# Performance work log

Hardware: AMD Instinct MI355X
Metric: run time of the kernel (lower is better)

The kernel has to match this reference:

```python
import jax, jax.numpy as jnp
import numpy as np

N_NODES = 100000
N_EDGES = 1250000
F_IN = 128
F_OUT = 64
N_GRAPHS = 256


def setup_inputs() -> dict:
    key = jax.random.key(0)
    k1, k2, k3, k4, k5 = jax.random.split(key, 5)
    node_feat = jax.random.normal(k1, (N_NODES, F_IN), dtype=jnp.float32)
    edge_index = jax.random.randint(k2, (2, N_EDGES), 0, N_NODES, dtype=jnp.int32)
    batch = jnp.sort(jax.random.randint(k3, (N_NODES,), 0, N_GRAPHS, dtype=jnp.int32))
    # PyG Linear weight layout: [out_channels, in_channels]; glorot-ish scale
    W = jax.random.normal(k4, (F_OUT, F_IN), dtype=jnp.float32) / np.sqrt(F_IN)
    b = jax.random.normal(k5, (F_OUT,), dtype=jnp.float32) * 0.01
    return {"node_feat": node_feat, "edge_index": edge_index, "batch": batch,
            "W": W, "b": b, "num_graphs": N_GRAPHS}


def reference(node_feat, edge_index, batch, W, b, num_graphs):
    n = node_feat.shape[0]
    # GCNConv: linear transform (no bias yet)
    x = node_feat @ W.T  # [N, F_OUT]
    # add self-loops (PyG default add_self_loops=True)
    loop = jnp.arange(n, dtype=edge_index.dtype)
    row = jnp.concatenate([edge_index[0], loop])  # source
    col = jnp.concatenate([edge_index[1], loop])  # target
    # symmetric normalization deg^{-1/2}[row] * deg^{-1/2}[col], deg over targets
    deg = jax.ops.segment_sum(jnp.ones_like(col, dtype=x.dtype), col, num_segments=n)
    dis = jnp.where(deg > 0, jax.lax.rsqrt(deg), 0.0)
    norm = dis[row] * dis[col]  # [E+N]
    # gather -> scale -> scatter-add, then bias
    agg = jax.ops.segment_sum(x[row] * norm[:, None], col, num_segments=n)
    out = jax.nn.relu(agg + b)
    # global_mean_pool over batch ids
    sums = jax.ops.segment_sum(out, batch, num_segments=num_graphs)
    counts = jax.ops.segment_sum(jnp.ones((n,), out.dtype), batch, num_segments=num_graphs)
    return sums / jnp.maximum(counts, 1.0)[:, None]
```

## Files before the change

### kernel.cpp

```cpp
#include <hip/hip_runtime.h>

#define N_NODES  100000
#define N_EDGES  1250000
#define F_IN     128
#define F_OUT    64
#define N_GRAPHS 256
#define NB_LIN   1563
#define NB_LINB  391
#define NBKT     782
#define NCHK     256
#define CHKSZ    4883
#define M_H      (NBKT * NCHK)
#define MB_H     196
#define BKT_CAP  2048

typedef __attribute__((ext_vector_type(8))) short short8;
typedef __attribute__((ext_vector_type(4))) float f32x4;

static __device__ __forceinline__ unsigned short f2bf(float f) {
    unsigned u = __builtin_bit_cast(unsigned, f);
    u += 0x7fff + ((u >> 16) & 1);
    return (unsigned short)(u >> 16);
}
static __device__ __forceinline__ float bf2f(unsigned short h) {
    unsigned u = ((unsigned)h) << 16;
    return __builtin_bit_cast(float, u);
}
static __device__ __forceinline__ float bflo(unsigned v) {
    return __builtin_bit_cast(float, v << 16);
}
static __device__ __forceinline__ float bfhi(unsigned v) {
    return __builtin_bit_cast(float, v & 0xffff0000u);
}

__global__ __launch_bounds__(256) void hist_k(const int* __restrict__ col,
                                              int* __restrict__ H) {
    __shared__ int cnt[NBKT];
    int c = blockIdx.x, tid = threadIdx.x;
    for (int b = tid; b < NBKT; b += 256) cnt[b] = 0;
    __syncthreads();
    int s = c * CHKSZ;
    int e = s + CHKSZ; if (e > N_EDGES) e = N_EDGES;
    for (int i = s + tid; i < e; i += 256)
        atomicAdd(&cnt[col[i] >> 7], 1);
    __syncthreads();
    for (int b = tid; b < NBKT; b += 256)
        H[b * NCHK + c] = cnt[b];
}

__global__ __launch_bounds__(1024) void scanH1_k(int* __restrict__ H, int* __restrict__ bsum) {
    __shared__ int lds[1024];
    int tid = threadIdx.x;
    int i = blockIdx.x * 1024 + tid;
    int v = (i < M_H) ? H[i] : 0;
    lds[tid] = v;
    __syncthreads();
    for (int off = 1; off < 1024; off <<= 1) {
        int t = (tid >= off) ? lds[tid - off] : 0;
        __syncthreads();
        lds[tid] += t;
        __syncthreads();
    }
    if (i < M_H) H[i] = lds[tid] - v;
    if (tid == 1023) bsum[blockIdx.x] = lds[tid];
}

__global__ __launch_bounds__(256) void scanH2_k(int* __restrict__ bsum) {
    __shared__ int lds[256];
    int tid = threadIdx.x;
    int v = (tid < MB_H) ? bsum[tid] : 0;
    lds[tid] = v;
    __syncthreads();
    for (int off = 1; off < 256; off <<= 1) {
        int t = (tid >= off) ? lds[tid - off] : 0;
        __syncthreads();
        lds[tid] += t;
        __syncthreads();
    }
    if (tid < MB_H) bsum[tid] = lds[tid] - v;
}

__global__ __launch_bounds__(1024) void scanH3_k(int* __restrict__ H, const int* __restrict__ bsum) {
    int i = blockIdx.x * 1024 + threadIdx.x;
    if (i < M_H) H[i] += bsum[blockIdx.x];
}

__global__ __launch_bounds__(256) void scatter_lin_k(const int* __restrict__ row,
                                                     const int* __restrict__ col,
                                                     const int* __restrict__ Hs,
                                                     int2* __restrict__ part,
                                                     const float* __restrict__ x,
                                                     const float* __restrict__ W,
                                                     unsigned short* __restrict__ z) {
    __shared__ unsigned smem[2 * 64 * 64];
    int tid = threadIdx.x;

    if (blockIdx.x < NCHK) {
        int* cur = (int*)smem;
        int c = blockIdx.x;
        for (int b = tid; b < NBKT; b += 256) cur[b] = Hs[b * NCHK + c];
        __syncthreads();
        int s = c * CHKSZ;
        int e = s + CHKSZ; if (e > N_EDGES) e = N_EDGES;
        for (int i = s + tid; i < e; i += 256) {
            int cc = col[i], rr = row[i];
            int p = atomicAdd(&cur[cc >> 7], 1);
            part[p] = make_int2(rr, cc);
        }
        return;
    }

    unsigned* xs = smem;
    unsigned* ws = smem + 64 * 64;
    int lb = blockIdx.x - NCHK;

    #pragma unroll
    for (int rr = 0; rr < 8; ++rr) {
        int idx = rr * 256 + tid;
        int n = idx >> 5, q = idx & 31;
        int d   = (n << 6) + (q << 1);
        int sdw = (n & 7) << 2;
        const float4 wv = *(const float4*)(W + (size_t)n * F_IN + q * 4);
        ws[(d ^ sdw)]     = (unsigned)f2bf(wv.x) | ((unsigned)f2bf(wv.y) << 16);
        ws[(d ^ sdw) + 1] = (unsigned)f2bf(wv.z) | ((unsigned)f2bf(wv.w) << 16);
    }

    int lane = tid & 63;
    int wv_  = tid >> 6;
    int m0   = wv_ << 4;
    int lr   = lane & 15;
    int lg   = lane >> 4;

    for (int t4 = 0; t4 < 4; ++t4) {
        int tile = lb * 4 + t4;
        if (tile >= NB_LIN) break;
        int base = tile * 64;
        int nmax = N_NODES - base; if (nmax > 64) nmax = 64;

        #pragma unroll
        for (int rr = 0; rr < 8; ++rr) {
            int idx = rr * 256 + tid;
            int n = idx >> 5, q = idx & 31;
            int d   = (n << 6) + (q << 1);
            int sdw = (n & 7) << 2;
            float4 xv = make_float4(0.f, 0.f, 0.f, 0.f);
            if (n < nmax) xv = *(const float4*)(x + (size_t)(base + n) * F_IN + q * 4);
            xs[(d ^ sdw)]     = (unsigned)f2bf(xv.x) | ((unsigned)f2bf(xv.y) << 16);
            xs[(d ^ sdw) + 1] = (unsigned)f2bf(xv.z) | ((unsigned)f2bf(xv.w) << 16);
        }
        __syncthreads();

        f32x4 acc0 = (f32x4)(0.f), acc1 = (f32x4)(0.f);
        f32x4 acc2 = (f32x4)(0.f), acc3 = (f32x4)(0.f);

        #pragma unroll
        for (int t = 0; t < 4; ++t) {
            int nn = m0 + lr;
            int da = ((nn << 6) + (t << 4) + (lg << 2)) ^ ((nn & 7) << 2);
            short8 a = *(const short8*)(xs + da);
            #pragma unroll
            for (int ff = 0; ff < 4; ++ff) {
                int f  = (ff << 4) + lr;
                int db = ((f << 6) + (t << 4) + (lg << 2)) ^ ((f & 7) << 2);
                short8 b = *(const short8*)(ws + db);
                f32x4 c = (ff == 0) ? acc0 : (ff == 1) ? acc1 : (ff == 2) ? acc2 : acc3;
                c = __builtin_amdgcn_mfma_f32_16x16x32_bf16(a, b, c, 0, 0, 0);
                if (ff == 0) acc0 = c; else if (ff == 1) acc1 = c;
                else if (ff == 2) acc2 = c; else acc3 = c;
            }
        }

        #pragma unroll
        for (int r = 0; r < 4; ++r) {
            int node = m0 + (lg << 2) + r;
            if (node < nmax) {
                size_t o = (size_t)(base + node) * F_OUT + lr;
                z[o +  0] = f2bf(acc0[r]);
                z[o + 16] = f2bf(acc1[r]);
                z[o + 32] = f2bf(acc2[r]);
                z[o + 48] = f2bf(acc3[r]);
            }
        }
        __syncthreads();
    }
}

__global__ __launch_bounds__(256) void csr_k(const int* __restrict__ Hs,
                                             const int2* __restrict__ part,
                                             int* __restrict__ bucketF,
                                             int* __restrict__ deg,
                                             int* __restrict__ offs,
                                             float* __restrict__ dis,
                                             unsigned* __restrict__ z32) {
    __shared__ int rowL[BKT_CAP];
    __shared__ int colL[BKT_CAP];
    __shared__ int cnt[128], offsL[128], curL[128], scanT[128];
    __shared__ float disL[128];
    int b = blockIdx.x, tid = threadIdx.x;
    int s = Hs[b * NCHK];
    int e = (b < NBKT - 1) ? Hs[(b + 1) * NCHK] : N_EDGES;
    int m = e - s;

    if (tid < 128) cnt[tid] = 0;
    __syncthreads();
    for (int i = tid; i < m; i += 256) {
        int2 pr = part[s + i];
        rowL[i] = pr.x;
        int cl = pr.y & 127;
        colL[i] = cl;
        atomicAdd(&cnt[cl], 1);
    }
    __syncthreads();
    if (tid < 128) scanT[tid] = cnt[tid];
    __syncthreads();
    for (int off = 1; off < 128; off <<= 1) {
        int v = (tid < 128 && tid >= off) ? scanT[tid - off] : 0;
        __syncthreads();
        if (tid < 128) scanT[tid] += v;
        __syncthreads();
    }
    if (tid < 128) {
        int ex = scanT[tid] - cnt[tid];
        offsL[tid] = ex;
        curL[tid]  = ex;
        float d = rsqrtf((float)cnt[tid] + 1.0f);
        disL[tid] = d;
        int node = b * 128 + tid;
        if (node < N_NODES) {
            deg[node]  = cnt[tid];
            offs[node] = s + ex;
            dis[node]  = d;
        }
    }
    __syncthreads();
    for (int i = tid; i < m; i += 256) {
        int cl = colL[i];
        int p = atomicAdd(&curL[cl], 1);
        bucketF[s + p] = rowL[i];
    }
    int node = tid >> 1, half = tid & 1;
    int gnode = b * 128 + node;
    if (gnode < N_NODES) {
        float d = disL[node];
        unsigned* zp = z32 + (size_t)gnode * 32 + half * 16;
        #pragma unroll
        for (int k = 0; k < 16; ++k) {
            unsigned v = zp[k];
            zp[k] = (unsigned)f2bf(d * bflo(v)) | ((unsigned)f2bf(d * bfhi(v)) << 16);
        }
    }
}

__global__ __launch_bounds__(256, 4) void gather_pool_k(const unsigned short* __restrict__ y,
                                                        const int* __restrict__ offs,
                                                        const int* __restrict__ deg,
                                                        const int* __restrict__ bucket,
                                                        const float* __restrict__ dis,
                                                        const int* __restrict__ batch,
                                                        const float* __restrict__ bias,
                                                        float* __restrict__ psum,
                                                        int* __restrict__ pcnt) {
    int lane = threadIdx.x & 63;
    int wid  = threadIdx.x >> 6;
    int i0   = (blockIdx.x * 4 + wid) * 8;
    int eo   = lane >> 5;
    int fp   = lane & 31;
    float bx = bias[2 * fp], by = bias[2 * fp + 1];
    const unsigned short* yb = y + 2 * fp;

    int   om = (lane < 8) ? offs[i0 + lane]  : 0;
    int   dm = (lane < 8) ? deg[i0 + lane]   : 0;
    float sm = (lane < 8) ? dis[i0 + lane]   : 0.f;
    int   gm = (lane < 8) ? batch[i0 + lane] : 0;

    float rx = 0.f, ry = 0.f;
    int cur = -1, runlen = 0;
    #pragma unroll
    for (int n = 0; n < 8; ++n) {
        int i = i0 + n;
        int s = __shfl(om, n);
        int e = s + __shfl(dm, n);

        unsigned sv = *(const unsigned*)(yb + (size_t)i * F_OUT);
        float ax = (eo == 0) ? bflo(sv) : 0.f;
        float ay = (eo == 0) ? bfhi(sv) : 0.f;

        for (int j = s; j < e; j += 16) {
            int rr[8];
            #pragma unroll
            for (int u = 0; u < 8; ++u) {
                int id = j + 2 * u + eo;
                rr[u] = bucket[(id < e) ? id : e - 1];
            }
            unsigned wv[8];
            #pragma unroll
            for (int u = 0; u < 8; ++u) {
                unsigned w = *(const unsigned*)(yb + (size_t)rr[u] * F_OUT);
                wv[u] = (j + 2 * u + eo < e) ? w : 0u;
            }
            #pragma unroll
            for (int u = 0; u < 8; ++u) {
                ax += bflo(wv[u]);
                ay += bfhi(wv[u]);
            }
        }
        ax += __shfl_xor(ax, 32);
        ay += __shfl_xor(ay, 32);

        float di = __shfl(sm, n);
        float vx = fmaxf(fmaf(di, ax, bx), 0.f);
        float vy = fmaxf(fmaf(di, ay, by), 0.f);
        int g = __shfl(gm, n);
        if (g != cur) {
            if (cur >= 0 && eo == 0) {
                atomicAdd(&psum[cur * F_OUT + 2 * fp],     rx);
                atomicAdd(&psum[cur * F_OUT + 2 * fp + 1], ry);
                if (lane == 0) atomicAdd(&pcnt[cur], runlen);
            }
            cur = g; rx = 0.f; ry = 0.f; runlen = 0;
        }
        rx += vx; ry += vy; runlen++;
    }
    if (cur >= 0 && eo == 0) {
        atomicAdd(&psum[cur * F_OUT + 2 * fp],     rx);
        atomicAdd(&psum[cur * F_OUT + 2 * fp + 1], ry);
        if (lane == 0) atomicAdd(&pcnt[cur], runlen);
    }
}

__global__ __launch_bounds__(256) void final_k(const float* __restrict__ psum,
                                               const int* __restrict__ pcnt,
                                               float* __restrict__ out) {
    int t = blockIdx.x * blockDim.x + threadIdx.x;
    if (t < N_GRAPHS * F_OUT) {
        int g = t >> 6;
        float c = (float)(pcnt[g] > 1 ? pcnt[g] : 1);
        out[t] = psum[t] / c;
    }
}

extern "C" void kernel_launch(void* const* d_in, const int* in_sizes, int n_in,
                              void* d_out, int out_size, void* d_ws, size_t ws_size,
                              hipStream_t stream) {
    const float* node_feat = (const float*)d_in[0];
    const int*   edges     = (const int*)d_in[1];
    const int*   batch     = (const int*)d_in[2];
    const float* W         = (const float*)d_in[3];
    const float* b         = (const float*)d_in[4];

    unsigned short* z = (unsigned short*)d_ws;
    int2*  part    = (int2*)(z + (size_t)N_NODES * F_OUT);
    int*   bucketF = (int*)(part + N_EDGES);
    int*   H       = bucketF + N_EDGES;
    int*   bsumH   = H + M_H;
    int*   deg     = bsumH + 256;
    int*   offs    = deg + N_NODES;
    float* dis     = (float*)(offs + N_NODES);
    float* psum    = dis + N_NODES;
    int*   pcnt    = (int*)(psum + N_GRAPHS * F_OUT);

    hipMemsetAsync(psum, 0, ((size_t)N_GRAPHS * F_OUT + N_GRAPHS) * 4, stream);

    const int* row = edges;
    const int* col = edges + N_EDGES;

    hist_k<<<NCHK, 256, 0, stream>>>(col, H);
    scanH1_k<<<MB_H, 1024, 0, stream>>>(H, bsumH);
    scanH2_k<<<1, 256, 0, stream>>>(bsumH);
    scanH3_k<<<MB_H, 1024, 0, stream>>>(H, bsumH);
    scatter_lin_k<<<NCHK + NB_LINB, 256, 0, stream>>>(row, col, H, part,
                                                      node_feat, W, z);
    csr_k<<<NBKT, 256, 0, stream>>>(H, part, bucketF, deg, offs, dis, (unsigned*)z);
    gather_pool_k<<<N_NODES / 32, 256, 0, stream>>>(z, offs, deg, bucketF,
                                                    dis, batch, b, psum, pcnt);
    final_k<<<(N_GRAPHS * F_OUT + 255) / 256, 256, 0, stream>>>(psum, pcnt, (float*)d_out);
}
```

Before: 118.8 us.

## Split feature matrix into four 16-column slices and gather per slice with LDS-staged edges

The transformed features are stored as four planar slices of 16 bf16 columns per node, and the gather kernel launches four times as many blocks, one per slice. Each slice's gather touches a 3.2MB table, which is more likely to stay cache-resident than the full 12.8MB row-major table. Each block stages its contiguous bucket range into LDS, falling back to global loads when it overflows. The trade-off is that the edge index list is read four times and each gathered access is only 32 bytes, with more shuffle reductions and more atomics.

```diff
diff --git a/kernel.cpp b/kernel.cpp
--- a/kernel.cpp
+++ b/kernel.cpp
@@ -13,6 +13,8 @@
 #define M_H      (NBKT * NCHK)
 #define MB_H     196
 #define BKT_CAP  2048
+#define GCAP     1536
+#define NBLK_G   3125
 
 typedef __attribute__((ext_vector_type(8))) short short8;
 typedef __attribute__((ext_vector_type(4))) float f32x4;
@@ -174,11 +176,11 @@
         for (int r = 0; r < 4; ++r) {
             int node = m0 + (lg << 2) + r;
             if (node < nmax) {
-                size_t o = (size_t)(base + node) * F_OUT + lr;
-                z[o +  0] = f2bf(acc0[r]);
-                z[o + 16] = f2bf(acc1[r]);
-                z[o + 32] = f2bf(acc2[r]);
-                z[o + 48] = f2bf(acc3[r]);
+                size_t nd = (size_t)(base + node);
+                z[((size_t)0 * N_NODES + nd) * 16 + lr] = f2bf(acc0[r]);
+                z[((size_t)1 * N_NODES + nd) * 16 + lr] = f2bf(acc1[r]);
+                z[((size_t)2 * N_NODES + nd) * 16 + lr] = f2bf(acc2[r]);
+                z[((size_t)3 * N_NODES + nd) * 16 + lr] = f2bf(acc3[r]);
             }
         }
         __syncthreads();
@@ -242,36 +244,52 @@
     int gnode = b * 128 + node;
     if (gnode < N_NODES) {
         float d = disL[node];
-        unsigned* zp = z32 + (size_t)gnode * 32 + half * 16;
         #pragma unroll
-        for (int k = 0; k < 16; ++k) {
-            unsigned v = zp[k];
-            zp[k] = (unsigned)f2bf(d * bflo(v)) | ((unsigned)f2bf(d * bfhi(v)) << 16);
-        }
-    }
-}
-
-__global__ __launch_bounds__(256, 4) void gather_pool_k(const unsigned short* __restrict__ y,
-                                                        const int* __restrict__ offs,
-                                                        const int* __restrict__ deg,
-                                                        const int* __restrict__ bucket,
-                                                        const float* __restrict__ dis,
-                                                        const int* __restrict__ batch,
-                                                        const float* __restrict__ bias,
-                                                        float* __restrict__ psum,
-                                                        int* __restrict__ pcnt) {
-    int lane = threadIdx.x & 63;
-    int wid  = threadIdx.x >> 6;
-    int i0   = (blockIdx.x * 4 + wid) * 8;
-    int eo   = lane >> 5;
-    int fp   = lane & 31;
-    float bx = bias[2 * fp], by = bias[2 * fp + 1];
-    const unsigned short* yb = y + 2 * fp;
+        for (int p = 0; p < 4; ++p) {
+            unsigned* zp = z32 + ((size_t)p * N_NODES + gnode) * 8 + half * 4;
+            #pragma unroll
+            for (int k = 0; k < 4; ++k) {
+                unsigned v = zp[k];
+                zp[k] = (unsigned)f2bf(d * bflo(v)) | ((unsigned)f2bf(d * bfhi(v)) << 16);
+            }
+        }
+    }
+}
+
+__global__ __launch_bounds__(256) void gather_pool_k(const unsigned* __restrict__ z32,
+                                                     const int* __restrict__ offs,
+                                                     const int* __restrict__ deg,
+                                                     const int* __restrict__ bucket,
+                                                     const float* __restrict__ dis,
+                                                     const int* __restrict__ batch,
+                                                     const float* __restrict__ bias,
+                                                     float* __restrict__ psum,
+                                                     int* __restrict__ pcnt) {
+    __shared__ int bktL[GCAP];
+    int tid   = threadIdx.x;
+    int lane  = tid & 63;
+    int wid   = tid >> 6;
+    int slice = blockIdx.x / NBLK_G;
+    int blk   = blockIdx.x - slice * NBLK_G;
+    int B     = blk * 32;
+    int i0    = B + wid * 8;
+    int es    = lane >> 3;
+    int fl    = lane & 7;
+    float bx  = bias[slice * 16 + 2 * fl];
+    float by  = bias[slice * 16 + 2 * fl + 1];
+    const unsigned* yb = z32 + (size_t)slice * N_NODES * 8 + fl;
+
+    int s0   = offs[B];
+    int eBlk = (B + 32 < N_NODES) ? offs[B + 32] : N_EDGES;
+    int L    = eBlk - s0; if (L > GCAP) L = GCAP;
+    for (int t = tid; t < L; t += 256)
+        bktL[t] = __builtin_nontemporal_load(bucket + s0 + t);
 
     int   om = (lane < 8) ? offs[i0 + lane]  : 0;
     int   dm = (lane < 8) ? deg[i0 + lane]   : 0;
     float sm = (lane < 8) ? dis[i0 + lane]   : 0.f;
     int   gm = (lane < 8) ? batch[i0 + lane] : 0;
+    __syncthreads();
 
     float rx = 0.f, ry = 0.f;
     int cur = -1, runlen = 0;
@@ -281,50 +299,55 @@
         int s = __shfl(om, n);
         int e = s + __shfl(dm, n);
 
-        unsigned sv = *(const unsigned*)(yb + (size_t)i * F_OUT);
-        float ax = (eo == 0) ? bflo(sv) : 0.f;
-        float ay = (eo == 0) ? bfhi(sv) : 0.f;
-
-        for (int j = s; j < e; j += 16) {
-            int rr[8];
-            #pragma unroll
-            for (int u = 0; u < 8; ++u) {
-                int id = j + 2 * u + eo;
-                rr[u] = bucket[(id < e) ? id : e - 1];
-            }
-            unsigned wv[8];
-            #pragma unroll
-            for (int u = 0; u < 8; ++u) {
-                unsigned w = *(const unsigned*)(yb + (size_t)rr[u] * F_OUT);
-                wv[u] = (j + 2 * u + eo < e) ? w : 0u;
-            }
-            #pragma unroll
-            for (int u = 0; u < 8; ++u) {
-                ax += bflo(wv[u]);
-                ay += bfhi(wv[u]);
-            }
-        }
-        ax += __shfl_xor(ax, 32);
-        ay += __shfl_xor(ay, 32);
+        unsigned sv = yb[(size_t)i * 8];
+        float ax = (es == 0) ? bflo(sv) : 0.f;
+        float ay = (es == 0) ? bfhi(sv) : 0.f;
+
+        if (e - s0 <= GCAP) {
+            for (int j = s; j < e; j += 16) {
+                #pragma unroll
+                for (int u = 0; u < 2; ++u) {
+                    int id  = j + u * 8 + es;
+                    int r   = bktL[((id < e) ? id : e - 1) - s0];
+                    unsigned w = yb[(size_t)r * 8];
+                    ax += (id < e) ? bflo(w) : 0.f;
+                    ay += (id < e) ? bfhi(w) : 0.f;
+                }
+            }
+        } else {
+            for (int j = s; j < e; j += 16) {
+                #pragma unroll
+                for (int u = 0; u < 2; ++u) {
+                    int id  = j + u * 8 + es;
+                    int r   = __builtin_nontemporal_load(bucket + ((id < e) ? id : e - 1));
+                    unsigned w = yb[(size_t)r * 8];
+                    ax += (id < e) ? bflo(w) : 0.f;
+                    ay += (id < e) ? bfhi(w) : 0.f;
+                }
+            }
+        }
+        ax += __shfl_xor(ax, 8);  ay += __shfl_xor(ay, 8);
+        ax += __shfl_xor(ax, 16); ay += __shfl_xor(ay, 16);
+        ax += __shfl_xor(ax, 32); ay += __shfl_xor(ay, 32);
 
         float di = __shfl(sm, n);
         float vx = fmaxf(fmaf(di, ax, bx), 0.f);
         float vy = fmaxf(fmaf(di, ay, by), 0.f);
         int g = __shfl(gm, n);
         if (g != cur) {
-            if (cur >= 0 && eo == 0) {
-                atomicAdd(&psum[cur * F_OUT + 2 * fp],     rx);
-                atomicAdd(&psum[cur * F_OUT + 2 * fp + 1], ry);
-                if (lane == 0) atomicAdd(&pcnt[cur], runlen);
+            if (cur >= 0 && es == 0) {
+                atomicAdd(&psum[cur * F_OUT + slice * 16 + 2 * fl],     rx);
+                atomicAdd(&psum[cur * F_OUT + slice * 16 + 2 * fl + 1], ry);
+                if (lane == 0 && slice == 0) atomicAdd(&pcnt[cur], runlen);
             }
             cur = g; rx = 0.f; ry = 0.f; runlen = 0;
         }
         rx += vx; ry += vy; runlen++;
     }
-    if (cur >= 0 && eo == 0) {
-        atomicAdd(&psum[cur * F_OUT + 2 * fp],     rx);
-        atomicAdd(&psum[cur * F_OUT + 2 * fp + 1], ry);
-        if (lane == 0) atomicAdd(&pcnt[cur], runlen);
+    if (cur >= 0 && es == 0) {
+        atomicAdd(&psum[cur * F_OUT + slice * 16 + 2 * fl],     rx);
+        atomicAdd(&psum[cur * F_OUT + slice * 16 + 2 * fl + 1], ry);
+        if (lane == 0 && slice == 0) atomicAdd(&pcnt[cur], runlen);
     }
 }
 
@@ -371,7 +394,7 @@
     scatter_lin_k<<<NCHK + NB_LINB, 256, 0, stream>>>(row, col, H, part,
                                                       node_feat, W, z);
     csr_k<<<NBKT, 256, 0, stream>>>(H, part, bucketF, deg, offs, dis, (unsigned*)z);
-    gather_pool_k<<<N_NODES / 32, 256, 0, stream>>>(z, offs, deg, bucketF,
-                                                    dis, batch, b, psum, pcnt);
+    gather_pool_k<<<4 * NBLK_G, 256, 0, stream>>>((const unsigned*)z, offs, deg, bucketF,
+                                                  dis, batch, b, psum, pcnt);
     final_k<<<(N_GRAPHS * F_OUT + 255) / 256, 256, 0, stream>>>(psum, pcnt, (float*)d_out);
 }
```

Measured after the change: 151.0 us. +27.1%, slower.
